# Kernel optimization log

Measured on AMD Instinct MI355X. Metric: run time of the kernel, lower is better.

## Reference

```python
import jax, jax.numpy as jnp
import numpy as np

H = 2048          # hidden_size
NH = 16           # num_attention_heads
D = H // NH       # head dim = 128
FFN = 4 * H       # mlp hidden
EPS = 1e-5
NORM = float(np.sqrt(D))  # coeff=max(1,layer_number)=1 cancels in FusedScaleMaskSoftmax
NEG = -10000.0    # attention_mask_func fill value
L2EPS = 1e-12     # F.normalize eps


def layernorm(x, g, b):
    m = jnp.mean(x, axis=-1, keepdims=True)
    v = jnp.var(x, axis=-1, keepdims=True)
    return (x - m) * jax.lax.rsqrt(v + EPS) * g + b


def l2norm(x):
    n = jnp.sqrt(jnp.sum(x * x, axis=-1, keepdims=True))
    return x / jnp.maximum(n, L2EPS)


def mlp(x, w1, b1, w2, b2):
    # GPT MLP with skip_bias_add: returns (h@w2, bias)
    h = jax.nn.gelu(x @ w1 + b1, approximate=False)
    return h @ w2, b2


def setup_inputs():
    S, B, M = 2048, 2, 4096
    key = jax.random.key(0)
    ks = jax.random.split(key, 12)
    r = lambda i, shape: jax.random.normal(ks[i], shape, jnp.float32) * 0.02
    return {
        'x': jax.random.normal(ks[0], (S, B, H), jnp.float32),
        'past_hidden': jax.random.normal(ks[1], (M, B, H), jnp.float32),
        'mem_mask': jax.random.randint(ks[2], (B, 1, S, M), 0, 2) == 1,
        'ln1_g': jnp.ones((H,), jnp.float32), 'ln1_b': jnp.zeros((H,), jnp.float32),
        'ln2_g': jnp.ones((H,), jnp.float32), 'ln2_b': jnp.zeros((H,), jnp.float32),
        'ln3_g': jnp.ones((H,), jnp.float32), 'ln3_b': jnp.zeros((H,), jnp.float32),
        'mlp1_w1': r(3, (H, FFN)), 'mlp1_b1': jnp.zeros((FFN,), jnp.float32),
        'mlp1_w2': r(4, (FFN, H)), 'mlp1_b2': jnp.zeros((H,), jnp.float32),
        'mlp2_w1': r(5, (H, FFN)), 'mlp2_b1': jnp.zeros((FFN,), jnp.float32),
        'mlp2_w2': r(6, (FFN, H)), 'mlp2_b2': jnp.zeros((H,), jnp.float32),
        'wq': r(7, (H, H)), 'bq': jnp.zeros((H,), jnp.float32),
        'wkv': r(8, (H, 2 * H)), 'bkv': jnp.zeros((2 * H,), jnp.float32),
        'wd': r(9, (H, H)), 'bd': jnp.zeros((H,), jnp.float32),
    }


def reference(x, past_hidden, mem_mask, ln1_g, ln1_b, ln2_g, ln2_b, ln3_g, ln3_b,
              mlp1_w1, mlp1_b1, mlp1_w2, mlp1_b2, mlp2_w1, mlp2_b1, mlp2_w2, mlp2_b2,
              wq, bq, wkv, bkv, wd, bd):
    S, B, _ = x.shape
    M = past_hidden.shape[0]

    # mlp1 branch (output replaces x, residual is NOT added for mlp1 per source)
    o1, bias1 = mlp(layernorm(x, ln1_g, ln1_b), mlp1_w1, mlp1_b1, mlp1_w2, mlp1_b2)
    x = o1 + bias1

    # memory attention
    h = layernorm(x, ln2_g, ln2_b)
    q = l2norm((h @ wq + bq).reshape(S, B, NH, D))            # [S,B,NH,D]
    kv = (past_hidden @ wkv + bkv).reshape(M, B, NH, 2 * D)   # [M,B,NH,2D]
    k = l2norm(kv[..., :D])
    v = l2norm(kv[..., D:])
    scores = jnp.einsum('sbhd,mbhd->bhsm', q, k) / NORM       # [B,NH,S,M]
    scores = jnp.where(mem_mask, NEG, scores.astype(jnp.float32))
    probs = jax.nn.softmax(scores, axis=-1).astype(q.dtype)
    ctx = jnp.einsum('bhsm,mbhd->sbhd', probs, v).reshape(S, B, H)
    x = x + ctx @ wd + bd

    # mlp2 branch with residual
    o2, bias2 = mlp(layernorm(x, ln3_g, ln3_b), mlp2_w1, mlp2_b1, mlp2_w2, mlp2_b2)
    return x + o2 + bias2
```

## Files before the change

### kernel.cpp

```cpp
#include <hip/hip_runtime.h>


typedef unsigned short ushort_t;
typedef __attribute__((ext_vector_type(8))) short bf16x8;
typedef __attribute__((ext_vector_type(4))) float f32x4;

#define DEVI __device__ __forceinline__

DEVI ushort_t f2bf(float f) {
  unsigned int u = __builtin_bit_cast(unsigned int, f);
  u += 0x7FFFu + ((u >> 16) & 1u);
  return (ushort_t)(u >> 16);
}
DEVI float bf2f(ushort_t h) {
  unsigned int u = ((unsigned int)h) << 16;
  return __builtin_bit_cast(float, u);
}

DEVI void load_lds16(const void* g, void* l) {
  __builtin_amdgcn_global_load_lds(
      (__attribute__((address_space(1))) void*)(g),
      (__attribute__((address_space(3))) void*)(l), 16, 0, 0);
}

__global__ void detect_mask_k(const unsigned int* __restrict__ m, int* __restrict__ flag) {
  unsigned int v = m[threadIdx.x];
  unsigned long long ok = __ballot(v <= 1u);
  if (threadIdx.x == 0) *flag = (ok == ~0ull) ? 1 : 0;
}

__global__ __launch_bounds__(256)
void mask_pack_k(const void* __restrict__ maskp, const int* __restrict__ mtype,
                 unsigned long long* __restrict__ out, int nwords) {
  const int mint = *mtype;
  const int lane = threadIdx.x & 63;
  const int wglob = blockIdx.x * 4 + (threadIdx.x >> 6);
  const int nw = gridDim.x * 4;
  const unsigned char* m8 = (const unsigned char*)maskp;
  const int* m32 = (const int*)maskp;
  for (int i = wglob; i < nwords; i += nw) {
    const size_t e = (size_t)i * 64 + lane;
    const bool v = mint ? (m32[e] != 0) : (m8[e] != 0);
    unsigned long long bits = __ballot(v);
    if (lane == 0) out[i] = bits;
  }
}

__global__ __launch_bounds__(256)
void transpose_w(const float* __restrict__ in, ushort_t* __restrict__ out, int K, int N) {
  __shared__ float t[32][33];
  const int tx = threadIdx.x, ty = threadIdx.y;
  const int n0 = blockIdx.x * 32, k0 = blockIdx.y * 32;
#pragma unroll
  for (int i = 0; i < 4; ++i)
    t[ty + i * 8][tx] = in[(size_t)(k0 + ty + i * 8) * N + n0 + tx];
  __syncthreads();
#pragma unroll
  for (int i = 0; i < 4; ++i)
    out[(size_t)(n0 + ty + i * 8) * K + k0 + tx] = f2bf(t[tx][ty + i * 8]);
}

__global__ void f32_to_bf16_k(const float* __restrict__ in, ushort_t* __restrict__ out, int n4) {
  int i = blockIdx.x * blockDim.x + threadIdx.x;
  int stride = gridDim.x * blockDim.x;
  for (; i < n4; i += stride) {
    float4 v = ((const float4*)in)[i];
    ushort4 o;
    o.x = f2bf(v.x); o.y = f2bf(v.y); o.z = f2bf(v.z); o.w = f2bf(v.w);
    ((ushort4*)out)[i] = o;
  }
}

__global__ __launch_bounds__(256)
void ln_kernel(const float* __restrict__ in, const float* __restrict__ gam,
               const float* __restrict__ bet, ushort_t* __restrict__ out) {
  const int row = blockIdx.x;
  const float* p = in + (size_t)row * 2048;
  const int tid = threadIdx.x;
  float4 v0 = ((const float4*)p)[tid * 2];
  float4 v1 = ((const float4*)p)[tid * 2 + 1];
  float s = v0.x + v0.y + v0.z + v0.w + v1.x + v1.y + v1.z + v1.w;
  float q = v0.x * v0.x + v0.y * v0.y + v0.z * v0.z + v0.w * v0.w +
            v1.x * v1.x + v1.y * v1.y + v1.z * v1.z + v1.w * v1.w;
#pragma unroll
  for (int m = 1; m < 64; m <<= 1) { s += __shfl_xor(s, m); q += __shfl_xor(q, m); }
  __shared__ float red[8];
  const int w = tid >> 6;
  if ((tid & 63) == 0) { red[w] = s; red[4 + w] = q; }
  __syncthreads();
  s = red[0] + red[1] + red[2] + red[3];
  q = red[4] + red[5] + red[6] + red[7];
  const float mean = s * (1.f / 2048.f);
  const float var = q * (1.f / 2048.f) - mean * mean;
  const float rs = rsqrtf(var + 1e-5f);
  float4 g0 = ((const float4*)gam)[tid * 2], g1 = ((const float4*)gam)[tid * 2 + 1];
  float4 b0 = ((const float4*)bet)[tid * 2], b1 = ((const float4*)bet)[tid * 2 + 1];
  ushort4 o0, o1;
  o0.x = f2bf((v0.x - mean) * rs * g0.x + b0.x);
  o0.y = f2bf((v0.y - mean) * rs * g0.y + b0.y);
  o0.z = f2bf((v0.z - mean) * rs * g0.z + b0.z);
  o0.w = f2bf((v0.w - mean) * rs * g0.w + b0.w);
  o1.x = f2bf((v1.x - mean) * rs * g1.x + b1.x);
  o1.y = f2bf((v1.y - mean) * rs * g1.y + b1.y);
  o1.z = f2bf((v1.z - mean) * rs * g1.z + b1.z);
  o1.w = f2bf((v1.w - mean) * rs * g1.w + b1.w);
  ushort4* ob = (ushort4*)(out + (size_t)row * 2048);
  ob[tid * 2] = o0;
  ob[tid * 2 + 1] = o1;
}

__global__ __launch_bounds__(256)
void vtrans_k(const ushort_t* __restrict__ kv, ushort_t* __restrict__ vt) {
  __shared__ ushort_t t[32][33];
  const int tx = threadIdx.x, ty = threadIdx.y;
  const int m0 = blockIdx.x * 32, d0 = blockIdx.y * 32, bh = blockIdx.z;
  const int b = bh >> 4, h = bh & 15;
#pragma unroll
  for (int i = 0; i < 4; ++i)
    t[ty + i * 8][tx] = kv[((size_t)(m0 + ty + i * 8) * 2 + b) * 4096 + h * 256 + 128 + d0 + tx];
  __syncthreads();
#pragma unroll
  for (int i = 0; i < 4; ++i)
    vt[((size_t)bh * 128 + d0 + ty + i * 8) * 4096 + m0 + tx] = t[tx][ty + i * 8];
}

template <int EPI>
__global__ __launch_bounds__(256, 3)
void gemm_s(const ushort_t* __restrict__ A, const ushort_t* __restrict__ Bt,
            const float* __restrict__ bias, const float* __restrict__ Xres,
            void* __restrict__ Out, int N, int K, int GM, float nscale) {
  __shared__ ushort_t lA[128 * 64];
  __shared__ ushort_t lB[128 * 64];

  const int tid = threadIdx.x;
  const int lane = tid & 63;
  const int w = tid >> 6;
  const int l15 = lane & 15, lhi = lane >> 4;
  const int wr = w >> 1, wc = w & 1;

  const int nwg = gridDim.x;
  const int cpx = nwg >> 3;
  const int swz = (blockIdx.x & 7) * cpx + (blockIdx.x >> 3);
  const int tm = swz % GM, tn = swz / GM;

  size_t aSrc[4], bSrc[4];
#pragma unroll
  for (int i = 0; i < 4; ++i) {
    const int ch = i * 256 + tid;
    const int row = ch >> 3;
    const int colb = ((ch & 7) * 16) ^ ((row & 7) << 4);
    aSrc[i] = (size_t)(tm * 128 + row) * K + (colb >> 1);
    bSrc[i] = (size_t)(tn * 128 + row) * K + (colb >> 1);
  }

  f32x4 acc[4][4] = {};

  const int KT = K >> 6;
  for (int kt = 0; kt < KT; ++kt) {
    const int k0 = kt << 6;
#pragma unroll
    for (int i = 0; i < 4; ++i) {
      load_lds16(A + aSrc[i] + k0, (char*)lA + (i * 256 + tid) * 16);
      load_lds16(Bt + bSrc[i] + k0, (char*)lB + (i * 256 + tid) * 16);
    }
    __syncthreads();
#pragma unroll
    for (int kk = 0; kk < 2; ++kk) {
      const int kb = kk * 64 + lhi * 16;
      bf16x8 bfr[4], af[4];
#pragma unroll
      for (int nf = 0; nf < 4; ++nf) {
        const int rb = wc * 64 + nf * 16 + l15;
        bfr[nf] = *(const bf16x8*)((const char*)lB + rb * 128 + (kb ^ ((rb & 7) << 4)));
      }
#pragma unroll
      for (int mf = 0; mf < 4; ++mf) {
        const int ra = wr * 64 + mf * 16 + l15;
        af[mf] = *(const bf16x8*)((const char*)lA + ra * 128 + (kb ^ ((ra & 7) << 4)));
      }
#pragma unroll
      for (int mf = 0; mf < 4; ++mf)
#pragma unroll
        for (int nf = 0; nf < 4; ++nf)
          acc[mf][nf] = __builtin_amdgcn_mfma_f32_16x16x32_bf16(af[mf], bfr[nf], acc[mf][nf], 0, 0, 0);
    }
    __syncthreads();
  }

  const int row0 = tm * 128 + wr * 64;
  const int col0 = tn * 128 + wc * 64;
  float bj[4];
#pragma unroll
  for (int nf = 0; nf < 4; ++nf) bj[nf] = bias[col0 + nf * 16 + l15];

  float inv_n[4][4];
  if constexpr (EPI == 4) {
    float part[4][4];
#pragma unroll
    for (int mf = 0; mf < 4; ++mf)
#pragma unroll
      for (int r = 0; r < 4; ++r) {
        float p = 0.f;
#pragma unroll
        for (int nf = 0; nf < 4; ++nf) {
          const float v = acc[mf][nf][r] + bj[nf];
          p += v * v;
        }
        part[mf][r] = p;
      }
#pragma unroll
    for (int ms = 1; ms < 16; ms <<= 1)
#pragma unroll
      for (int mf = 0; mf < 4; ++mf)
#pragma unroll
        for (int r = 0; r < 4; ++r) part[mf][r] += __shfl_xor(part[mf][r], ms);
    float* sq = (float*)lA;
    if (l15 == 0) {
#pragma unroll
      for (int mf = 0; mf < 4; ++mf)
#pragma unroll
        for (int r = 0; r < 4; ++r)
          sq[wc * 128 + wr * 64 + mf * 16 + lhi * 4 + r] = part[mf][r];
    }
    __syncthreads();
#pragma unroll
    for (int mf = 0; mf < 4; ++mf)
#pragma unroll
      for (int r = 0; r < 4; ++r) {
        const int idx = wr * 64 + mf * 16 + lhi * 4 + r;
        const float tot = sq[idx] + sq[128 + idx];
        inv_n[mf][r] = nscale / fmaxf(sqrtf(tot), 1e-12f);
      }
  }

#pragma unroll
  for (int mf = 0; mf < 4; ++mf) {
#pragma unroll
    for (int nf = 0; nf < 4; ++nf) {
      const int col = col0 + nf * 16 + l15;
#pragma unroll
      for (int r = 0; r < 4; ++r) {
        const int row = row0 + mf * 16 + lhi * 4 + r;
        const size_t idx = (size_t)row * N + col;
        float v = acc[mf][nf][r] + bj[nf];
        if constexpr (EPI == 0) {
          v = 0.5f * v * (1.f + erff(v * 0.70710678118654752f));
          ((ushort_t*)Out)[idx] = f2bf(v);
        } else if constexpr (EPI == 1) {
          ((ushort_t*)Out)[idx] = f2bf(v);
        } else if constexpr (EPI == 2) {
          ((float*)Out)[idx] = v;
        } else if constexpr (EPI == 3) {
          ((float*)Out)[idx] = Xres[idx] + v;
        } else {
          ((ushort_t*)Out)[idx] = f2bf(v * inv_n[mf][r]);
        }
      }
    }
  }
}

__global__ __launch_bounds__(512, 4)
void attn_k(const ushort_t* __restrict__ Q, const ushort_t* __restrict__ KV,
            const ushort_t* __restrict__ VT,
            const unsigned long long* __restrict__ PM,
            ushort_t* __restrict__ CTX) {
  __shared__ ushort_t lk[2][64 * 128];
  __shared__ ushort_t lvt[2][128 * 64];
  __shared__ ushort_t lp[8][16 * 64];

  const int tid = threadIdx.x, lane = tid & 63, w = tid >> 6;
  const int l15 = lane & 15, lhi = lane >> 4;
  const int wid = ((blockIdx.x & 7) << 6) + (blockIdx.x >> 3);
  const int qt = wid & 15, pair = wid >> 4;
  const int b = pair >> 4, h = pair & 15;

  size_t kSrc[2], vSrc[2];
  int kDst[2], vDst[2];
#pragma unroll
  for (int i = 0; i < 2; ++i) {
    const int ch = (i * 8 + w) * 64 + lane;
    {
      const int row = ch >> 4;
      const int cb = ((ch & 15) * 16) ^ ((row & 7) << 4);
      kSrc[i] = ((size_t)row * 2 + b) * 4096 + h * 256 + (cb >> 1);
      kDst[i] = (i * 8 + w) * 1024;
    }
    {
      const int row = ch >> 3;
      const int cb = ((ch & 7) * 16) ^ ((row & 7) << 4);
      vSrc[i] = (size_t)pair * 128 * 4096 + (size_t)row * 4096 + (cb >> 1);
      vDst[i] = (i * 8 + w) * 1024;
    }
  }

  bf16x8 aq[4];
  {
    const ushort_t* qbase =
        Q + ((size_t)(qt * 128 + w * 16 + l15) * 2 + b) * 2048 + h * 128 + lhi * 8;
#pragma unroll
    for (int kk = 0; kk < 4; ++kk) aq[kk] = *(const bf16x8*)(qbase + kk * 32);
  }

  float l_acc[4] = {0.f, 0.f, 0.f, 0.f};
  f32x4 acc_o[8] = {};
  const unsigned long long* mrow =
      PM + (size_t)(b * 2048 + qt * 128 + w * 16 + lhi * 4) * 64;
  const int l15p16 = l15 + 16;

#pragma unroll
  for (int i = 0; i < 2; ++i) {
    load_lds16(KV + kSrc[i], (char*)lk[0] + kDst[i]);
    load_lds16(VT + vSrc[i], (char*)lvt[0] + vDst[i]);
  }
  __syncthreads();

  int cur = 0;
  for (int t = 0; t < 64; ++t) {
    if (t < 63) {
      const size_t kAdd = (size_t)(t + 1) * 64 * 8192;
      const int vAdd = (t + 1) * 64;
#pragma unroll
      for (int i = 0; i < 2; ++i) {
        load_lds16(KV + kSrc[i] + kAdd, (char*)lk[cur ^ 1] + kDst[i]);
        load_lds16(VT + vSrc[i] + vAdd, (char*)lvt[cur ^ 1] + vDst[i]);
      }
    }
    unsigned long long mw[4];
#pragma unroll
    for (int r = 0; r < 4; ++r) mw[r] = mrow[r * 64 + t];

    f32x4 sa[4] = {};
#pragma unroll
    for (int kk = 0; kk < 4; ++kk) {
#pragma unroll
      for (int j = 0; j < 4; ++j) {
        const int krow = j * 16 + l15;
        const int bcb = (kk * 64 + lhi * 16) ^ ((krow & 7) << 4);
        bf16x8 bk = *(const bf16x8*)((const char*)lk[cur] + krow * 256 + bcb);
        sa[j] = __builtin_amdgcn_mfma_f32_16x16x32_bf16(aq[kk], bk, sa[j], 0, 0, 0);
      }
    }

#pragma unroll
    for (int r = 0; r < 4; ++r) {
      const unsigned int mlo = (unsigned int)mw[r];
      const unsigned int mhi = (unsigned int)(mw[r] >> 32);
#pragma unroll
      for (int j = 0; j < 4; ++j) {
        const unsigned int sel = (j < 2) ? mlo : mhi;
        const int sh = (j & 1) ? l15p16 : l15;
        const bool mk = (sel >> sh) & 1u;
        const float p = __expf(sa[j][r]);
        const float pv = mk ? 0.f : p;
        sa[j][r] = pv;
        l_acc[r] += pv;
      }
    }

#pragma unroll
    for (int r = 0; r < 4; ++r) {
      unsigned int pk0, pk1;
      asm("v_cvt_pk_bf16_f32 %0, %1, %2" : "=v"(pk0) : "v"(sa[0][r]), "v"(sa[1][r]));
      asm("v_cvt_pk_bf16_f32 %0, %1, %2" : "=v"(pk1) : "v"(sa[2][r]), "v"(sa[3][r]));
      const int prow = lhi * 4 + r;
      char* base = (char*)lp[w] + prow * 128;
      const int swz = (prow & 7) << 4;
      *(ushort_t*)(base + ((l15 * 2) ^ swz)) = (ushort_t)pk0;
      *(ushort_t*)(base + (((16 + l15) * 2) ^ swz)) = (ushort_t)(pk0 >> 16);
      *(ushort_t*)(base + (((32 + l15) * 2) ^ swz)) = (ushort_t)pk1;
      *(ushort_t*)(base + (((48 + l15) * 2) ^ swz)) = (ushort_t)(pk1 >> 16);
    }

#pragma unroll
    for (int ks = 0; ks < 2; ++ks) {
      const int acb2 = (ks * 64 + lhi * 16) ^ ((l15 & 7) << 4);
      bf16x8 ap = *(const bf16x8*)((const char*)lp[w] + l15 * 128 + acb2);
#pragma unroll
      for (int d = 0; d < 8; ++d) {
        const int vrow = d * 16 + l15;
        const int vcb = (ks * 64 + lhi * 16) ^ ((vrow & 7) << 4);
        bf16x8 bv = *(const bf16x8*)((const char*)lvt[cur] + vrow * 128 + vcb);
        acc_o[d] = __builtin_amdgcn_mfma_f32_16x16x32_bf16(ap, bv, acc_o[d], 0, 0, 0);
      }
    }
    __syncthreads();
    cur ^= 1;
  }

#pragma unroll
  for (int ms = 1; ms < 16; ms <<= 1)
#pragma unroll
    for (int r = 0; r < 4; ++r) l_acc[r] += __shfl_xor(l_acc[r], ms);

#pragma unroll
  for (int r = 0; r < 4; ++r) {
    const float inv = 1.f / fmaxf(l_acc[r], 1e-20f);
    const size_t orow = ((size_t)(qt * 128 + w * 16 + lhi * 4 + r) * 2 + b) * 2048 + h * 128;
#pragma unroll
    for (int d = 0; d < 8; ++d)
      CTX[orow + d * 16 + l15] = f2bf(acc_o[d][r] * inv);
  }
}

extern "C" void kernel_launch(void* const* d_in, const int* in_sizes, int n_in,
                              void* d_out, int out_size, void* d_ws, size_t ws_size,
                              hipStream_t stream) {
  (void)in_sizes; (void)n_in; (void)out_size; (void)ws_size;
  const float* x    = (const float*)d_in[0];
  const float* ph   = (const float*)d_in[1];
  const void*  mask = d_in[2];
  const float* ln1g = (const float*)d_in[3];
  const float* ln1b = (const float*)d_in[4];
  const float* ln2g = (const float*)d_in[5];
  const float* ln2b = (const float*)d_in[6];
  const float* ln3g = (const float*)d_in[7];
  const float* ln3b = (const float*)d_in[8];
  const float* w1a  = (const float*)d_in[9];
  const float* b1a  = (const float*)d_in[10];
  const float* w2a  = (const float*)d_in[11];
  const float* b2a  = (const float*)d_in[12];
  const float* w1b  = (const float*)d_in[13];
  const float* b1b  = (const float*)d_in[14];
  const float* w2b  = (const float*)d_in[15];
  const float* b2b  = (const float*)d_in[16];
  const float* wq   = (const float*)d_in[17];
  const float* bq   = (const float*)d_in[18];
  const float* wkv  = (const float*)d_in[19];
  const float* bkv  = (const float*)d_in[20];
  const float* wd   = (const float*)d_in[21];
  const float* bd   = (const float*)d_in[22];

  char* ws = (char*)d_ws;
  int* flag = (int*)ws;
  size_t off = 256;
  auto alloc = [&](size_t bytes) {
    void* p = ws + off;
    off += (bytes + 255) & ~(size_t)255;
    return p;
  };
  ushort_t* WT1   = (ushort_t*)alloc(2048ull * 8192 * 2);
  ushort_t* WT2   = (ushort_t*)alloc(2048ull * 8192 * 2);
  ushort_t* WQT   = (ushort_t*)alloc(2048ull * 2048 * 2);
  ushort_t* WKVT  = (ushort_t*)alloc(2048ull * 4096 * 2);
  ushort_t* WDT   = (ushort_t*)alloc(2048ull * 2048 * 2);
  ushort_t* H1    = (ushort_t*)alloc(4096ull * 2048 * 2);
  ushort_t* GELU  = (ushort_t*)alloc(4096ull * 8192 * 2);
  float*    X     = (float*)alloc(4096ull * 2048 * 4);
  ushort_t* QRAW  = (ushort_t*)alloc(4096ull * 2048 * 2);
  ushort_t* PH16  = (ushort_t*)alloc(8192ull * 2048 * 2);
  ushort_t* KVRAW = (ushort_t*)alloc(8192ull * 4096 * 2);
  ushort_t* VT    = PH16;
  ushort_t* CTX   = WKVT;
  unsigned long long* PMASK = (unsigned long long*)GELU;

  const dim3 tb(32, 8);
  const float SSCALE = 0.088388347648318447f;

  detect_mask_k<<<1, 64, 0, stream>>>((const unsigned int*)mask, flag);

  transpose_w<<<dim3(256, 64), tb, 0, stream>>>(w1a, WT1, 2048, 8192);
  transpose_w<<<dim3(64, 256), tb, 0, stream>>>(w2a, WT2, 8192, 2048);
  transpose_w<<<dim3(64, 64), tb, 0, stream>>>(wq, WQT, 2048, 2048);
  transpose_w<<<dim3(128, 64), tb, 0, stream>>>(wkv, WKVT, 2048, 4096);
  transpose_w<<<dim3(64, 64), tb, 0, stream>>>(wd, WDT, 2048, 2048);

  ln_kernel<<<4096, 256, 0, stream>>>(x, ln1g, ln1b, H1);
  gemm_s<0><<<2048, 256, 0, stream>>>(H1, WT1, b1a, nullptr, GELU, 8192, 2048, 32, 0.f);
  gemm_s<2><<<512, 256, 0, stream>>>(GELU, WT2, b2a, nullptr, X, 2048, 8192, 32, 0.f);

  mask_pack_k<<<1024, 256, 0, stream>>>(mask, flag, PMASK, 262144);

  ln_kernel<<<4096, 256, 0, stream>>>(X, ln2g, ln2b, H1);
  gemm_s<4><<<512, 256, 0, stream>>>(H1, WQT, bq, nullptr, QRAW, 2048, 2048, 32, SSCALE);
  f32_to_bf16_k<<<2048, 256, 0, stream>>>(ph, PH16, 8192 * 2048 / 4);
  gemm_s<4><<<2048, 256, 0, stream>>>(PH16, WKVT, bkv, nullptr, KVRAW, 4096, 2048, 64, 1.0f);
  vtrans_k<<<dim3(128, 4, 32), tb, 0, stream>>>(KVRAW, VT);
  attn_k<<<512, 512, 0, stream>>>(QRAW, KVRAW, VT, PMASK, CTX);
  gemm_s<3><<<512, 256, 0, stream>>>(CTX, WDT, bd, X, X, 2048, 2048, 32, 0.f);

  ln_kernel<<<4096, 256, 0, stream>>>(X, ln3g, ln3b, H1);
  transpose_w<<<dim3(256, 64), tb, 0, stream>>>(w1b, WT1, 2048, 8192);
  transpose_w<<<dim3(64, 256), tb, 0, stream>>>(w2b, WT2, 8192, 2048);
  gemm_s<0><<<2048, 256, 0, stream>>>(H1, WT1, b1b, nullptr, GELU, 8192, 2048, 32, 0.f);
  gemm_s<3><<<512, 256, 0, stream>>>(GELU, WT2, b2b, X, d_out, 2048, 8192, 32, 0.f);
}
```

Measured before the change: 1.329 ms.

## Add 256x256-tile 8-wave GEMM kernel for wide-N projections

Adds a new GEMM kernel using 512-thread workgroups and 256x256 output tiles. It splits each 64-wide K step into four staged quarter loads interleaved with MFMA phases, using double-buffered LDS, XOR-swizzled addressing, wave priority hints and an XCD-aware block swizzle. The kernel replaces the 128x128-tile GEMM for the two MLP up-projections and the KV projection, aiming for higher data reuse per tile and better overlap of loads with compute. The cost is larger LDS use (128KB) and higher register pressure from 8x4 accumulators, which limits occupancy. The bf16-only EPI==1 branch of the old GEMM is also removed.

Measured after the change: 1.714 ms. 29.0% more time.

```diff
diff --git a/kernel.cpp b/kernel.cpp
--- a/kernel.cpp
+++ b/kernel.cpp
@@ -21,6 +21,12 @@
   __builtin_amdgcn_global_load_lds(
       (__attribute__((address_space(1))) void*)(g),
       (__attribute__((address_space(3))) void*)(l), 16, 0, 0);
+}
+
+DEVI void pbar() {
+  asm volatile("" ::: "memory");
+  __builtin_amdgcn_s_barrier();
+  asm volatile("" ::: "memory");
 }
 
 __global__ void detect_mask_k(const unsigned int* __restrict__ m, int* __restrict__ flag) {
@@ -246,12 +252,209 @@
         if constexpr (EPI == 0) {
           v = 0.5f * v * (1.f + erff(v * 0.70710678118654752f));
           ((ushort_t*)Out)[idx] = f2bf(v);
-        } else if constexpr (EPI == 1) {
-          ((ushort_t*)Out)[idx] = f2bf(v);
         } else if constexpr (EPI == 2) {
           ((float*)Out)[idx] = v;
         } else if constexpr (EPI == 3) {
           ((float*)Out)[idx] = Xres[idx] + v;
+        } else {
+          ((ushort_t*)Out)[idx] = f2bf(v * inv_n[mf][r]);
+        }
+      }
+    }
+  }
+}
+
+template <int EPI>
+__global__ __launch_bounds__(512, 2)
+void gemm8(const ushort_t* __restrict__ A, const ushort_t* __restrict__ Bt,
+           const float* __restrict__ bias, void* __restrict__ Out,
+           int N, int K, int GM, float nscale) {
+  __shared__ ushort_t lA[2][256 * 64];
+  __shared__ ushort_t lB[2][256 * 64];
+
+  const int tid = threadIdx.x;
+  const int lane = tid & 63;
+  const int w = tid >> 6;
+  const int l15 = lane & 15, lhi = lane >> 4;
+  const int wr = w >> 2, wc = w & 3;
+
+  const int nwg = gridDim.x;
+  const int cpx = nwg >> 3;
+  const int swz = (blockIdx.x & 7) * cpx + (blockIdx.x >> 3);
+  const int tm = swz % GM, tn = swz / GM;
+
+  int srow[2], scolb[2], sch[2];
+  sch[0] = tid; sch[1] = 512 + tid;
+#pragma unroll
+  for (int i = 0; i < 2; ++i) {
+    srow[i] = sch[i] >> 3;
+    scolb[i] = ((sch[i] & 7) * 16) ^ ((srow[i] & 7) << 4);
+  }
+  auto stage = [&](int c, int buf, int k0) {
+    const int h = c & 1;
+    if (c >= 2) {
+#pragma unroll
+      for (int i = 0; i < 2; ++i)
+        load_lds16(A + (size_t)(tm * 256 + h * 128 + srow[i]) * K + k0 + (scolb[i] >> 1),
+                   (char*)lA[buf] + h * 16384 + sch[i] * 16);
+    } else {
+#pragma unroll
+      for (int i = 0; i < 2; ++i)
+        load_lds16(Bt + (size_t)(tn * 256 + h * 128 + srow[i]) * K + k0 + (scolb[i] >> 1),
+                   (char*)lB[buf] + h * 16384 + sch[i] * 16);
+    }
+  };
+
+  f32x4 acc[8][4] = {};
+  const int KT = K >> 6;
+
+  stage(0, 0, 0); stage(1, 0, 0); stage(2, 0, 0); stage(3, 0, 0);
+  asm volatile("s_waitcnt vmcnt(2)" ::: "memory");
+  pbar();
+
+  for (int kt = 0; kt < KT; ++kt) {
+    const int cur = kt & 1;
+    const bool more = (kt + 1) < KT;
+    const int k0n = (kt + 1) << 6;
+    const char* bA = (const char*)lA[cur];
+    const char* bB = (const char*)lB[cur];
+    bf16x8 bfr[2][4], af[4];
+
+    if (more) stage(0, cur ^ 1, k0n);
+#pragma unroll
+    for (int nf = 0; nf < 4; ++nf) {
+      const int rb = wc * 64 + nf * 16 + l15;
+      bfr[0][nf] = *(const bf16x8*)(bB + rb * 128 + ((lhi * 16) ^ ((rb & 7) << 4)));
+    }
+#pragma unroll
+    for (int mf = 0; mf < 4; ++mf) {
+      const int ra = wr * 64 + mf * 16 + l15;
+      af[mf] = *(const bf16x8*)(bA + ra * 128 + ((lhi * 16) ^ ((ra & 7) << 4)));
+    }
+    __builtin_amdgcn_s_setprio(1);
+#pragma unroll
+    for (int mf = 0; mf < 4; ++mf)
+#pragma unroll
+      for (int nf = 0; nf < 4; ++nf)
+        acc[mf][nf] = __builtin_amdgcn_mfma_f32_16x16x32_bf16(af[mf], bfr[0][nf], acc[mf][nf], 0, 0, 0);
+    __builtin_amdgcn_s_setprio(0);
+    pbar();
+
+    if (more) stage(1, cur ^ 1, k0n);
+#pragma unroll
+    for (int nf = 0; nf < 4; ++nf) {
+      const int rb = wc * 64 + nf * 16 + l15;
+      bfr[1][nf] = *(const bf16x8*)(bB + rb * 128 + ((64 + lhi * 16) ^ ((rb & 7) << 4)));
+    }
+#pragma unroll
+    for (int mf = 0; mf < 4; ++mf) {
+      const int ra = wr * 64 + mf * 16 + l15;
+      af[mf] = *(const bf16x8*)(bA + ra * 128 + ((64 + lhi * 16) ^ ((ra & 7) << 4)));
+    }
+    __builtin_amdgcn_s_setprio(1);
+#pragma unroll
+    for (int mf = 0; mf < 4; ++mf)
+#pragma unroll
+      for (int nf = 0; nf < 4; ++nf)
+        acc[mf][nf] = __builtin_amdgcn_mfma_f32_16x16x32_bf16(af[mf], bfr[1][nf], acc[mf][nf], 0, 0, 0);
+    __builtin_amdgcn_s_setprio(0);
+    if (more) asm volatile("s_waitcnt vmcnt(4)" ::: "memory");
+    else      asm volatile("s_waitcnt vmcnt(0)" ::: "memory");
+    pbar();
+
+    if (more) stage(2, cur ^ 1, k0n);
+#pragma unroll
+    for (int mf = 0; mf < 4; ++mf) {
+      const int ra = 128 + wr * 64 + mf * 16 + l15;
+      af[mf] = *(const bf16x8*)(bA + ra * 128 + ((lhi * 16) ^ ((ra & 7) << 4)));
+    }
+    __builtin_amdgcn_s_setprio(1);
+#pragma unroll
+    for (int mf = 0; mf < 4; ++mf)
+#pragma unroll
+      for (int nf = 0; nf < 4; ++nf)
+        acc[4 + mf][nf] = __builtin_amdgcn_mfma_f32_16x16x32_bf16(af[mf], bfr[0][nf], acc[4 + mf][nf], 0, 0, 0);
+    __builtin_amdgcn_s_setprio(0);
+    pbar();
+
+    if (more) stage(3, cur ^ 1, k0n);
+#pragma unroll
+    for (int mf = 0; mf < 4; ++mf) {
+      const int ra = 128 + wr * 64 + mf * 16 + l15;
+      af[mf] = *(const bf16x8*)(bA + ra * 128 + ((64 + lhi * 16) ^ ((ra & 7) << 4)));
+    }
+    __builtin_amdgcn_s_setprio(1);
+#pragma unroll
+    for (int mf = 0; mf < 4; ++mf)
+#pragma unroll
+      for (int nf = 0; nf < 4; ++nf)
+        acc[4 + mf][nf] = __builtin_amdgcn_mfma_f32_16x16x32_bf16(af[mf], bfr[1][nf], acc[4 + mf][nf], 0, 0, 0);
+    __builtin_amdgcn_s_setprio(0);
+    if (more) asm volatile("s_waitcnt vmcnt(2)" ::: "memory");
+    pbar();
+  }
+
+  const int col0 = tn * 256 + wc * 64;
+  float bj[4];
+#pragma unroll
+  for (int nf = 0; nf < 4; ++nf) bj[nf] = bias[col0 + nf * 16 + l15];
+
+  float inv_n[8][4];
+  if constexpr (EPI == 4) {
+    float* sq = (float*)lA;
+    float part[8][4];
+#pragma unroll
+    for (int mf = 0; mf < 8; ++mf)
+#pragma unroll
+      for (int r = 0; r < 4; ++r) {
+        float p = 0.f;
+#pragma unroll
+        for (int nf = 0; nf < 4; ++nf) {
+          const float v = acc[mf][nf][r] + bj[nf];
+          p += v * v;
+        }
+        part[mf][r] = p;
+      }
+#pragma unroll
+    for (int ms = 1; ms < 16; ms <<= 1)
+#pragma unroll
+      for (int mf = 0; mf < 8; ++mf)
+#pragma unroll
+        for (int r = 0; r < 4; ++r) part[mf][r] += __shfl_xor(part[mf][r], ms);
+    pbar();
+    if (l15 == 0) {
+#pragma unroll
+      for (int mf = 0; mf < 8; ++mf) {
+        const int absrow = (mf < 4 ? wr * 64 + mf * 16 : 128 + wr * 64 + (mf - 4) * 16) + lhi * 4;
+#pragma unroll
+        for (int r = 0; r < 4; ++r) sq[wc * 256 + absrow + r] = part[mf][r];
+      }
+    }
+    pbar();
+#pragma unroll
+    for (int mf = 0; mf < 8; ++mf) {
+      const int absrow = (mf < 4 ? wr * 64 + mf * 16 : 128 + wr * 64 + (mf - 4) * 16) + lhi * 4;
+#pragma unroll
+      for (int r = 0; r < 4; ++r) {
+        const float tot = sq[wc * 256 + absrow + r] + sq[(wc ^ 1) * 256 + absrow + r];
+        inv_n[mf][r] = nscale / fmaxf(sqrtf(tot), 1e-12f);
+      }
+    }
+  }
+
+#pragma unroll
+  for (int mf = 0; mf < 8; ++mf) {
+    const int rbase = tm * 256 + (mf < 4 ? wr * 64 + mf * 16 : 128 + wr * 64 + (mf - 4) * 16) + lhi * 4;
+#pragma unroll
+    for (int nf = 0; nf < 4; ++nf) {
+      const int col = col0 + nf * 16 + l15;
+#pragma unroll
+      for (int r = 0; r < 4; ++r) {
+        const size_t idx = (size_t)(rbase + r) * N + col;
+        float v = acc[mf][nf][r] + bj[nf];
+        if constexpr (EPI == 0) {
+          v = 0.5f * v * (1.f + erff(v * 0.70710678118654752f));
+          ((ushort_t*)Out)[idx] = f2bf(v);
         } else {
           ((ushort_t*)Out)[idx] = f2bf(v * inv_n[mf][r]);
         }
@@ -466,7 +669,7 @@
   transpose_w<<<dim3(64, 64), tb, 0, stream>>>(wd, WDT, 2048, 2048);
 
   ln_kernel<<<4096, 256, 0, stream>>>(x, ln1g, ln1b, H1);
-  gemm_s<0><<<2048, 256, 0, stream>>>(H1, WT1, b1a, nullptr, GELU, 8192, 2048, 32, 0.f);
+  gemm8<0><<<512, 512, 0, stream>>>(H1, WT1, b1a, GELU, 8192, 2048, 16, 0.f);
   gemm_s<2><<<512, 256, 0, stream>>>(GELU, WT2, b2a, nullptr, X, 2048, 8192, 32, 0.f);
 
   mask_pack_k<<<1024, 256, 0, stream>>>(mask, flag, PMASK, 262144);
@@ -474,7 +677,7 @@
   ln_kernel<<<4096, 256, 0, stream>>>(X, ln2g, ln2b, H1);
   gemm_s<4><<<512, 256, 0, stream>>>(H1, WQT, bq, nullptr, QRAW, 2048, 2048, 32, SSCALE);
   f32_to_bf16_k<<<2048, 256, 0, stream>>>(ph, PH16, 8192 * 2048 / 4);
-  gemm_s<4><<<2048, 256, 0, stream>>>(PH16, WKVT, bkv, nullptr, KVRAW, 4096, 2048, 64, 1.0f);
+  gemm8<4><<<512, 512, 0, stream>>>(PH16, WKVT, bkv, KVRAW, 4096, 2048, 32, 1.0f);
   vtrans_k<<<dim3(128, 4, 32), tb, 0, stream>>>(KVRAW, VT);
   attn_k<<<512, 512, 0, stream>>>(QRAW, KVRAW, VT, PMASK, CTX);
   gemm_s<3><<<512, 256, 0, stream>>>(CTX, WDT, bd, X, X, 2048, 2048, 32, 0.f);
@@ -482,6 +685,6 @@
   ln_kernel<<<4096, 256, 0, stream>>>(X, ln3g, ln3b, H1);
   transpose_w<<<dim3(256, 64), tb, 0, stream>>>(w1b, WT1, 2048, 8192);
   transpose_w<<<dim3(64, 256), tb, 0, stream>>>(w2b, WT2, 8192, 2048);
-  gemm_s<0><<<2048, 256, 0, stream>>>(H1, WT1, b1b, nullptr, GELU, 8192, 2048, 32, 0.f);
+  gemm8<0><<<512, 512, 0, stream>>>(H1, WT1, b1b, GELU, 8192, 2048, 16, 0.f);
   gemm_s<3><<<512, 256, 0, stream>>>(GELU, WT2, b2b, X, d_out, 2048, 8192, 32, 0.f);
 }
```
